# Optimization experiments

Hardware: AMD Instinct MI355X
Metric: run time of the kernel (lower is better)

The kernel has to match this reference:

```python
import jax, jax.numpy as jnp
import numpy as np

N_NODES = 50000
N_EDGES = 800000
D_FEAT = 64
THETA = [0.5, 0.3, 0.15, 0.05]  # polynomial filter coefficients, k = len(THETA)


def setup_inputs() -> dict:
    key = jax.random.key(0)
    k1, k2, k3 = jax.random.split(key, 3)
    feat = jax.random.normal(k1, (N_NODES, D_FEAT), dtype=jnp.float32)
    src = jax.random.randint(k2, (N_EDGES,), 0, N_NODES)  # A[src, dst] = 1
    dst = jax.random.randint(k3, (N_EDGES,), 0, N_NODES)
    return {"feat": feat, "src": src, "dst": dst}


def reference(feat, src, dst):
    # normalize_adj: D^{-1/2} A^T D^{-1/2} with D = rowsum(A) (inf -> 0 for isolated nodes).
    n = feat.shape[0]
    deg = jax.ops.segment_sum(jnp.ones(src.shape, dtype=feat.dtype), src, num_segments=n)
    d_inv_sqrt = jnp.where(deg > 0, jax.lax.rsqrt(jnp.maximum(deg, 1.0)), jnp.zeros_like(deg))
    # norm[i, j] = d_i^{-1/2} A[j, i] d_j^{-1/2}; edge (src=j, dst=i) carries weight
    w = d_inv_sqrt[src] * d_inv_sqrt[dst]  # [E]

    def spmm(x):
        # (A_norm @ x)[i] = sum over edges with dst==i of w_e * x[src_e]
        return jax.ops.segment_sum(w[:, None] * x[src], dst, num_segments=n)

    # Original loop: h = theta[0]*(A@f); for k>=1: f = A@f; h += theta[k]*f.
    # Note theta[0] and theta[1] both scale A@f0 (feat is not updated before h init),
    # so we fold them together and avoid recomputing the first SpMM.
    x = spmm(feat)  # A @ f0, shared by the k=0 and k=1 terms
    h = (THETA[0] + THETA[1]) * x
    for k in range(2, len(THETA)):
        x = spmm(x)
        h = h + THETA[k] * x
    return h
```

## Files before the change

kernel.cpp:

```cpp
#include <hip/hip_runtime.h>
#include <hip/hip_bf16.h>

#define N_NODES 50000
#define N_EDGES 800000
#define D_FEAT  64
#define NW      12500
#define G_SRC   64
#define G_DST   256
#define CONV_NB 128
#define FILL_NB 64
#define HB      512
#define SCAN_B  256
#define SCAN_NBLK ((NW + SCAN_B - 1) / SCAN_B)
#define CAP     48


typedef unsigned uint4_ev  __attribute__((ext_vector_type(4)));
typedef float    float4_ev __attribute__((ext_vector_type(4)));

__device__ __forceinline__ float bflo(unsigned u) { return __uint_as_float(u << 16); }
__device__ __forceinline__ float bfhi(unsigned u) { return __uint_as_float(u & 0xFFFF0000u); }
__device__ __forceinline__ unsigned pack_bf16(float a, float b) {
    __hip_bfloat16 x = __float2bfloat16(a), y = __float2bfloat16(b);
    unsigned short ux = *reinterpret_cast<unsigned short*>(&x);
    unsigned short uy = *reinterpret_cast<unsigned short*>(&y);
    return (unsigned)ux | ((unsigned)uy << 16);
}


__global__ void hist_cv_kernel(const int* __restrict__ src, const int* __restrict__ dst,
                               unsigned* __restrict__ psrc_p, unsigned* __restrict__ pdst_p,
                               const float* __restrict__ feat, unsigned* __restrict__ featbf,
                               unsigned* __restrict__ csr, int nE) {
    int t = threadIdx.x;
    int b = blockIdx.x;
    if (b >= G_SRC + G_DST + CONV_NB) {
        int fb = b - (G_SRC + G_DST + CONV_NB);
        uint4* c4 = (uint4*)csr;
        const int n4 = N_NODES * CAP / 4;
        const int nthr = FILL_NB * HB;
        uint4 z = make_uint4(0u, 0u, 0u, 0u);
        for (int i = fb * HB + t; i < n4; i += nthr) c4[i] = z;
        return;
    }
    if (b >= G_SRC + G_DST) {
        int cb = b - (G_SRC + G_DST);
        const float4* f4 = (const float4*)feat;
        uint2* fb2 = (uint2*)featbf;
        const int nthr = CONV_NB * HB;
        for (int i = cb * HB + t; i < N_NODES * 16; i += nthr) {
            float4 v = f4[i];
            fb2[i] = make_uint2(pack_bf16(v.x, v.y), pack_bf16(v.z, v.w));
        }
        return;
    }
    __shared__ unsigned bins[NW];
    for (int i = t; i < NW; i += HB) bins[i] = 0;
    __syncthreads();
    bool is_src = (b < G_SRC);
    int g = is_src ? b : (b - G_SRC);
    int nstr = is_src ? G_SRC : G_DST;
    const int4* k4 = (const int4*)(is_src ? src : dst);
    int nE4 = nE >> 2;
    for (int q = g * HB + t; q < nE4; q += nstr * HB) {
        int4 kv = k4[q];
        atomicAdd(&bins[kv.x >> 2], 1u << (8 * (kv.x & 3)));
        atomicAdd(&bins[kv.y >> 2], 1u << (8 * (kv.y & 3)));
        atomicAdd(&bins[kv.z >> 2], 1u << (8 * (kv.z & 3)));
        atomicAdd(&bins[kv.w >> 2], 1u << (8 * (kv.w & 3)));
    }
    __syncthreads();
    unsigned* p = (is_src ? psrc_p : pdst_p) + g * NW;
    for (int i = t; i < NW; i += HB) p[i] = bins[i];
}

__global__ void scanA_kernel(const unsigned* __restrict__ pdst_p, const unsigned* __restrict__ psrc_p,
                             unsigned* __restrict__ gbase_p, unsigned* __restrict__ deg_p,
                             float* __restrict__ dinv) {
    int w = blockIdx.x * SCAN_B + threadIdx.x;
    if (w >= NW) return;
    unsigned td = 0;
    #pragma unroll 16
    for (int g = 0; g < G_DST; g++) {
        gbase_p[g * NW + w] = td;
        td += pdst_p[g * NW + w];
    }
    deg_p[w] = td;
    unsigned ts = 0;
    #pragma unroll 16
    for (int g = 0; g < G_SRC; g++) ts += psrc_p[g * NW + w];
    unsigned d0 = ts & 255u, d1 = (ts >> 8) & 255u, d2 = (ts >> 16) & 255u, d3 = ts >> 24;
    float4 dv;
    dv.x = d0 ? rsqrtf((float)d0) : 0.0f;
    dv.y = d1 ? rsqrtf((float)d1) : 0.0f;
    dv.z = d2 ? rsqrtf((float)d2) : 0.0f;
    dv.w = d3 ? rsqrtf((float)d3) : 0.0f;
    ((float4*)dinv)[w] = dv;
}

__global__ void scatter_kernel(const int* __restrict__ src, const int* __restrict__ dst,
                               const unsigned* __restrict__ gbase_p, const float* __restrict__ dinv,
                               unsigned* __restrict__ csr, int nE) {
    __shared__ unsigned cur[NW];
    int t = threadIdx.x;
    int g = blockIdx.x;
    const unsigned* gb = gbase_p + (size_t)g * NW;
    for (int i = t; i < NW; i += HB) cur[i] = gb[i];
    __syncthreads();
    const int4* s4 = (const int4*)src;
    const int4* d4 = (const int4*)dst;
    int nE4 = nE >> 2;
    for (int q = g * HB + t; q < nE4; q += G_DST * HB) {
        int4 sv = s4[q];
        int4 dv = d4[q];
        {
            int k = dv.x; int sh = 8 * (k & 3);
            unsigned old = atomicAdd(&cur[k >> 2], 1u << sh);
            unsigned pw = __float2uint_rn(dinv[sv.x] * 32767.0f);
            csr[(size_t)k * CAP + ((old >> sh) & 255u)] = (pw << 17) | (unsigned)sv.x;
        }
        {
            int k = dv.y; int sh = 8 * (k & 3);
            unsigned old = atomicAdd(&cur[k >> 2], 1u << sh);
            unsigned pw = __float2uint_rn(dinv[sv.y] * 32767.0f);
            csr[(size_t)k * CAP + ((old >> sh) & 255u)] = (pw << 17) | (unsigned)sv.y;
        }
        {
            int k = dv.z; int sh = 8 * (k & 3);
            unsigned old = atomicAdd(&cur[k >> 2], 1u << sh);
            unsigned pw = __float2uint_rn(dinv[sv.z] * 32767.0f);
            csr[(size_t)k * CAP + ((old >> sh) & 255u)] = (pw << 17) | (unsigned)sv.z;
        }
        {
            int k = dv.w; int sh = 8 * (k & 3);
            unsigned old = atomicAdd(&cur[k >> 2], 1u << sh);
            unsigned pw = __float2uint_rn(dinv[sv.w] * 32767.0f);
            csr[(size_t)k * CAP + ((old >> sh) & 255u)] = (pw << 17) | (unsigned)sv.w;
        }
    }
}


struct Acc8 { float a0, a1, a2, a3, a4, a5, a6, a7; };

__device__ __forceinline__ Acc8 spmm_gather(int i, const unsigned* __restrict__ csr,
                                            const unsigned* __restrict__ x, unsigned deg,
                                            int eg, int c8) {
    const unsigned* row = csr + (size_t)i * CAP;
    const uint4* x4 = (const uint4*)x;
    const float WS = 1.0f / 32767.0f;
    unsigned v0 = __builtin_nontemporal_load(row + eg);
    unsigned v1 = __builtin_nontemporal_load(row + eg + 8);
    unsigned v2 = __builtin_nontemporal_load(row + eg + 16);
    int   s0 = (int)(v0 & 0x1FFFFu); float w0 = (float)(v0 >> 17) * WS;
    int   s1 = (int)(v1 & 0x1FFFFu); float w1 = (float)(v1 >> 17) * WS;
    int   s2 = (int)(v2 & 0x1FFFFu); float w2 = (float)(v2 >> 17) * WS;
    uint4 r0 = x4[(size_t)s0 * 8 + c8];
    uint4 r1 = x4[(size_t)s1 * 8 + c8];
    uint4 r2 = x4[(size_t)s2 * 8 + c8];
    float a0, a1, a2, a3, a4, a5, a6, a7;
    a0  = w0 * bflo(r0.x) + w1 * bflo(r1.x) + w2 * bflo(r2.x);
    a1  = w0 * bfhi(r0.x) + w1 * bfhi(r1.x) + w2 * bfhi(r2.x);
    a2  = w0 * bflo(r0.y) + w1 * bflo(r1.y) + w2 * bflo(r2.y);
    a3  = w0 * bfhi(r0.y) + w1 * bfhi(r1.y) + w2 * bfhi(r2.y);
    a4  = w0 * bflo(r0.z) + w1 * bflo(r1.z) + w2 * bflo(r2.z);
    a5  = w0 * bfhi(r0.z) + w1 * bfhi(r1.z) + w2 * bfhi(r2.z);
    a6  = w0 * bflo(r0.w) + w1 * bflo(r1.w) + w2 * bflo(r2.w);
    a7  = w0 * bfhi(r0.w) + w1 * bfhi(r1.w) + w2 * bfhi(r2.w);
    if (deg > 24) {
        unsigned v3 = __builtin_nontemporal_load(row + eg + 24);
        unsigned v4 = __builtin_nontemporal_load(row + eg + 32);
        unsigned v5 = __builtin_nontemporal_load(row + eg + 40);
        int   s3 = (int)(v3 & 0x1FFFFu); float w3 = (float)(v3 >> 17) * WS;
        int   s4 = (int)(v4 & 0x1FFFFu); float w4 = (float)(v4 >> 17) * WS;
        int   s5 = (int)(v5 & 0x1FFFFu); float w5 = (float)(v5 >> 17) * WS;
        uint4 r3 = x4[(size_t)s3 * 8 + c8];
        uint4 r4 = x4[(size_t)s4 * 8 + c8];
        uint4 r5 = x4[(size_t)s5 * 8 + c8];
        a0 += w3 * bflo(r3.x) + w4 * bflo(r4.x) + w5 * bflo(r5.x);
        a1 += w3 * bfhi(r3.x) + w4 * bfhi(r4.x) + w5 * bfhi(r5.x);
        a2 += w3 * bflo(r3.y) + w4 * bflo(r4.y) + w5 * bflo(r5.y);
        a3 += w3 * bfhi(r3.y) + w4 * bfhi(r4.y) + w5 * bfhi(r5.y);
        a4 += w3 * bflo(r3.z) + w4 * bflo(r4.z) + w5 * bflo(r5.z);
        a5 += w3 * bfhi(r3.z) + w4 * bfhi(r4.z) + w5 * bfhi(r5.z);
        a6 += w3 * bflo(r3.w) + w4 * bflo(r4.w) + w5 * bflo(r5.w);
        a7 += w3 * bfhi(r3.w) + w4 * bfhi(r4.w) + w5 * bfhi(r5.w);
    }
    #pragma unroll
    for (int d = 8; d <= 32; d <<= 1) {
        a0 += __shfl_xor(a0, d); a1 += __shfl_xor(a1, d);
        a2 += __shfl_xor(a2, d); a3 += __shfl_xor(a3, d);
        a4 += __shfl_xor(a4, d); a5 += __shfl_xor(a5, d);
        a6 += __shfl_xor(a6, d); a7 += __shfl_xor(a7, d);
    }
    Acc8 r = {a0, a1, a2, a3, a4, a5, a6, a7};
    return r;
}

__device__ __forceinline__ unsigned get_deg(const unsigned* __restrict__ deg_p, int i) {
    return (deg_p[(unsigned)i >> 2] >> (8 * (i & 3))) & 255u;
}

__global__ void spmm_mid_kernel(const unsigned* __restrict__ csr, const unsigned* __restrict__ deg_p,
                                const float* __restrict__ dinv,
                                const unsigned* __restrict__ x, unsigned* __restrict__ y) {
    int i = (blockIdx.x * blockDim.x + threadIdx.x) >> 6;
    if (i >= N_NODES) return;
    int lane = threadIdx.x & 63;
    unsigned deg = get_deg(deg_p, i);
    Acc8 A = spmm_gather(i, csr, x, deg, lane >> 3, lane & 7);
    if (lane < 8) {
        float di = dinv[i];
        uint4_ev p;
        p.x = pack_bf16(A.a0 * di, A.a1 * di);
        p.y = pack_bf16(A.a2 * di, A.a3 * di);
        p.z = pack_bf16(A.a4 * di, A.a5 * di);
        p.w = pack_bf16(A.a6 * di, A.a7 * di);
        __builtin_nontemporal_store(p, (uint4_ev*)y + (size_t)i * 8 + lane);
    }
}

__global__ void spmm_final_kernel(const unsigned* __restrict__ csr, const unsigned* __restrict__ deg_p,
                                  const float* __restrict__ dinv,
                                  const unsigned* __restrict__ x1, const unsigned* __restrict__ x2,
                                  float* __restrict__ h) {
    int i = (blockIdx.x * blockDim.x + threadIdx.x) >> 6;
    if (i >= N_NODES) return;
    int lane = threadIdx.x & 63;
    unsigned deg = get_deg(deg_p, i);
    Acc8 A = spmm_gather(i, csr, x2, deg, lane >> 3, lane & 7);
    if (lane < 8) {
        int c8 = lane;
        float di = dinv[i] * 0.05f;
        uint4 u1 = ((const uint4*)x1)[(size_t)i * 8 + c8];
        uint4 u2 = ((const uint4*)x2)[(size_t)i * 8 + c8];
        float4_ev o0, o1;
        o0.x = 0.8f * bflo(u1.x) + 0.15f * bflo(u2.x) + di * A.a0;
        o0.y = 0.8f * bfhi(u1.x) + 0.15f * bfhi(u2.x) + di * A.a1;
        o0.z = 0.8f * bflo(u1.y) + 0.15f * bflo(u2.y) + di * A.a2;
        o0.w = 0.8f * bfhi(u1.y) + 0.15f * bfhi(u2.y) + di * A.a3;
        o1.x = 0.8f * bflo(u1.z) + 0.15f * bflo(u2.z) + di * A.a4;
        o1.y = 0.8f * bfhi(u1.z) + 0.15f * bfhi(u2.z) + di * A.a5;
        o1.z = 0.8f * bflo(u1.w) + 0.15f * bflo(u2.w) + di * A.a6;
        o1.w = 0.8f * bfhi(u1.w) + 0.15f * bfhi(u2.w) + di * A.a7;
        float* hp = h + (size_t)i * 64 + c8 * 8;
        __builtin_nontemporal_store(o0, (float4_ev*)hp);
        __builtin_nontemporal_store(o1, (float4_ev*)(hp + 4));
    }
}


extern "C" void kernel_launch(void* const* d_in, const int* in_sizes, int n_in,
                              void* d_out, int out_size, void* d_ws, size_t ws_size,
                              hipStream_t stream) {
    const float* feat = (const float*)d_in[0];
    const int*   src  = (const int*)d_in[1];
    const int*   dst  = (const int*)d_in[2];
    float* h = (float*)d_out;

    char* ws = (char*)d_ws;
    unsigned* psrc_p   = (unsigned*)(ws);
    unsigned* pdst_p   = (unsigned*)(ws +  3200000u);
    unsigned* gbase_p  = (unsigned*)(ws + 16000000u);
    float*    dinv     = (float*)   (ws + 28800000u);
    unsigned* csr      = (unsigned*)(ws + 29000192u);
    unsigned* featbf   = (unsigned*)(ws + 38600192u);
    unsigned* bufA     = (unsigned*)(ws + 45000192u);
    unsigned* bufB     = (unsigned*)(ws + 51400192u);
    unsigned* deg_p    = (unsigned*)(ws + 57800192u);

    const int nE = N_EDGES;
    const int B = 256;

    hist_cv_kernel<<<G_SRC + G_DST + CONV_NB + FILL_NB, HB, 0, stream>>>(
        src, dst, psrc_p, pdst_p, feat, featbf, csr, nE);

    scanA_kernel<<<SCAN_NBLK, SCAN_B, 0, stream>>>(pdst_p, psrc_p, gbase_p, deg_p, dinv);

    scatter_kernel<<<G_DST, HB, 0, stream>>>(src, dst, gbase_p, dinv, csr, nE);

    const int spmmGrid = (N_NODES * 64 + B - 1) / B;
    spmm_mid_kernel<<<spmmGrid, B, 0, stream>>>(csr, deg_p, dinv, featbf, bufA);
    spmm_mid_kernel<<<spmmGrid, B, 0, stream>>>(csr, deg_p, dinv, bufA, bufB);
    spmm_final_kernel<<<spmmGrid, B, 0, stream>>>(csr, deg_p, dinv, bufA, bufB, h);
}
```

Baseline: 160.0 us.

## Map eight rows per wavefront with serial edge loop instead of one row

```diff
diff --git a/kernel.cpp b/kernel.cpp
--- a/kernel.cpp
+++ b/kernel.cpp
@@ -141,82 +141,67 @@
 }
 
 
+__device__ __forceinline__ unsigned get_deg(const unsigned* __restrict__ deg_p, int i) {
+    return (deg_p[(unsigned)i >> 2] >> (8 * (i & 3))) & 255u;
+}
+
 struct Acc8 { float a0, a1, a2, a3, a4, a5, a6, a7; };
 
-__device__ __forceinline__ Acc8 spmm_gather(int i, const unsigned* __restrict__ csr,
-                                            const unsigned* __restrict__ x, unsigned deg,
-                                            int eg, int c8) {
-    const unsigned* row = csr + (size_t)i * CAP;
+__device__ __forceinline__ Acc8 spmm_accum(int ii, int mdr, const unsigned* __restrict__ csr,
+                                           const unsigned* __restrict__ x, int c8) {
+    const unsigned* row = csr + (size_t)ii * CAP;
     const uint4* x4 = (const uint4*)x;
     const float WS = 1.0f / 32767.0f;
-    unsigned v0 = __builtin_nontemporal_load(row + eg);
-    unsigned v1 = __builtin_nontemporal_load(row + eg + 8);
-    unsigned v2 = __builtin_nontemporal_load(row + eg + 16);
-    int   s0 = (int)(v0 & 0x1FFFFu); float w0 = (float)(v0 >> 17) * WS;
-    int   s1 = (int)(v1 & 0x1FFFFu); float w1 = (float)(v1 >> 17) * WS;
-    int   s2 = (int)(v2 & 0x1FFFFu); float w2 = (float)(v2 >> 17) * WS;
-    uint4 r0 = x4[(size_t)s0 * 8 + c8];
-    uint4 r1 = x4[(size_t)s1 * 8 + c8];
-    uint4 r2 = x4[(size_t)s2 * 8 + c8];
-    float a0, a1, a2, a3, a4, a5, a6, a7;
-    a0  = w0 * bflo(r0.x) + w1 * bflo(r1.x) + w2 * bflo(r2.x);
-    a1  = w0 * bfhi(r0.x) + w1 * bfhi(r1.x) + w2 * bfhi(r2.x);
-    a2  = w0 * bflo(r0.y) + w1 * bflo(r1.y) + w2 * bflo(r2.y);
-    a3  = w0 * bfhi(r0.y) + w1 * bfhi(r1.y) + w2 * bfhi(r2.y);
-    a4  = w0 * bflo(r0.z) + w1 * bflo(r1.z) + w2 * bflo(r2.z);
-    a5  = w0 * bfhi(r0.z) + w1 * bfhi(r1.z) + w2 * bfhi(r2.z);
-    a6  = w0 * bflo(r0.w) + w1 * bflo(r1.w) + w2 * bflo(r2.w);
-    a7  = w0 * bfhi(r0.w) + w1 * bfhi(r1.w) + w2 * bfhi(r2.w);
-    if (deg > 24) {
-        unsigned v3 = __builtin_nontemporal_load(row + eg + 24);
-        unsigned v4 = __builtin_nontemporal_load(row + eg + 32);
-        unsigned v5 = __builtin_nontemporal_load(row + eg + 40);
+    float a0 = 0, a1 = 0, a2 = 0, a3 = 0, a4 = 0, a5 = 0, a6 = 0, a7 = 0;
+    for (int s = 0; s < mdr; s += 4) {
+        unsigned v0 = __builtin_nontemporal_load(row + s);
+        unsigned v1 = __builtin_nontemporal_load(row + s + 1);
+        unsigned v2 = __builtin_nontemporal_load(row + s + 2);
+        unsigned v3 = __builtin_nontemporal_load(row + s + 3);
+        int   s0 = (int)(v0 & 0x1FFFFu); float w0 = (float)(v0 >> 17) * WS;
+        int   s1 = (int)(v1 & 0x1FFFFu); float w1 = (float)(v1 >> 17) * WS;
+        int   s2 = (int)(v2 & 0x1FFFFu); float w2 = (float)(v2 >> 17) * WS;
         int   s3 = (int)(v3 & 0x1FFFFu); float w3 = (float)(v3 >> 17) * WS;
-        int   s4 = (int)(v4 & 0x1FFFFu); float w4 = (float)(v4 >> 17) * WS;
-        int   s5 = (int)(v5 & 0x1FFFFu); float w5 = (float)(v5 >> 17) * WS;
+        uint4 r0 = x4[(size_t)s0 * 8 + c8];
+        uint4 r1 = x4[(size_t)s1 * 8 + c8];
+        uint4 r2 = x4[(size_t)s2 * 8 + c8];
         uint4 r3 = x4[(size_t)s3 * 8 + c8];
-        uint4 r4 = x4[(size_t)s4 * 8 + c8];
-        uint4 r5 = x4[(size_t)s5 * 8 + c8];
-        a0 += w3 * bflo(r3.x) + w4 * bflo(r4.x) + w5 * bflo(r5.x);
-        a1 += w3 * bfhi(r3.x) + w4 * bfhi(r4.x) + w5 * bfhi(r5.x);
-        a2 += w3 * bflo(r3.y) + w4 * bflo(r4.y) + w5 * bflo(r5.y);
-        a3 += w3 * bfhi(r3.y) + w4 * bfhi(r4.y) + w5 * bfhi(r5.y);
-        a4 += w3 * bflo(r3.z) + w4 * bflo(r4.z) + w5 * bflo(r5.z);
-        a5 += w3 * bfhi(r3.z) + w4 * bfhi(r4.z) + w5 * bfhi(r5.z);
-        a6 += w3 * bflo(r3.w) + w4 * bflo(r4.w) + w5 * bflo(r5.w);
-        a7 += w3 * bfhi(r3.w) + w4 * bfhi(r4.w) + w5 * bfhi(r5.w);
-    }
-    #pragma unroll
-    for (int d = 8; d <= 32; d <<= 1) {
-        a0 += __shfl_xor(a0, d); a1 += __shfl_xor(a1, d);
-        a2 += __shfl_xor(a2, d); a3 += __shfl_xor(a3, d);
-        a4 += __shfl_xor(a4, d); a5 += __shfl_xor(a5, d);
-        a6 += __shfl_xor(a6, d); a7 += __shfl_xor(a7, d);
+        a0 += w0 * bflo(r0.x) + w1 * bflo(r1.x) + w2 * bflo(r2.x) + w3 * bflo(r3.x);
+        a1 += w0 * bfhi(r0.x) + w1 * bfhi(r1.x) + w2 * bfhi(r2.x) + w3 * bfhi(r3.x);
+        a2 += w0 * bflo(r0.y) + w1 * bflo(r1.y) + w2 * bflo(r2.y) + w3 * bflo(r3.y);
+        a3 += w0 * bfhi(r0.y) + w1 * bfhi(r1.y) + w2 * bfhi(r2.y) + w3 * bfhi(r3.y);
+        a4 += w0 * bflo(r0.z) + w1 * bflo(r1.z) + w2 * bflo(r2.z) + w3 * bflo(r3.z);
+        a5 += w0 * bfhi(r0.z) + w1 * bfhi(r1.z) + w2 * bfhi(r2.z) + w3 * bfhi(r3.z);
+        a6 += w0 * bflo(r0.w) + w1 * bflo(r1.w) + w2 * bflo(r2.w) + w3 * bflo(r3.w);
+        a7 += w0 * bfhi(r0.w) + w1 * bfhi(r1.w) + w2 * bfhi(r2.w) + w3 * bfhi(r3.w);
     }
     Acc8 r = {a0, a1, a2, a3, a4, a5, a6, a7};
     return r;
-}
-
-__device__ __forceinline__ unsigned get_deg(const unsigned* __restrict__ deg_p, int i) {
-    return (deg_p[(unsigned)i >> 2] >> (8 * (i & 3))) & 255u;
 }
 
 __global__ void spmm_mid_kernel(const unsigned* __restrict__ csr, const unsigned* __restrict__ deg_p,
                                 const float* __restrict__ dinv,
                                 const unsigned* __restrict__ x, unsigned* __restrict__ y) {
-    int i = (blockIdx.x * blockDim.x + threadIdx.x) >> 6;
-    if (i >= N_NODES) return;
+    int tid = blockIdx.x * blockDim.x + threadIdx.x;
     int lane = threadIdx.x & 63;
-    unsigned deg = get_deg(deg_p, i);
-    Acc8 A = spmm_gather(i, csr, x, deg, lane >> 3, lane & 7);
-    if (lane < 8) {
+    int g = lane >> 3, c8 = lane & 7;
+    int i = (tid >> 6) * 8 + g;
+    bool valid = i < N_NODES;
+    int ii = valid ? i : 0;
+    int md = valid ? (int)get_deg(deg_p, ii) : 0;
+    md = max(md, __shfl_xor(md, 8));
+    md = max(md, __shfl_xor(md, 16));
+    md = max(md, __shfl_xor(md, 32));
+    int mdr = (md + 3) & ~3;
+    Acc8 A = spmm_accum(ii, mdr, csr, x, c8);
+    if (valid) {
         float di = dinv[i];
         uint4_ev p;
         p.x = pack_bf16(A.a0 * di, A.a1 * di);
         p.y = pack_bf16(A.a2 * di, A.a3 * di);
         p.z = pack_bf16(A.a4 * di, A.a5 * di);
         p.w = pack_bf16(A.a6 * di, A.a7 * di);
-        __builtin_nontemporal_store(p, (uint4_ev*)y + (size_t)i * 8 + lane);
+        __builtin_nontemporal_store(p, (uint4_ev*)y + (size_t)i * 8 + c8);
     }
 }
 
@@ -224,13 +209,19 @@
                                   const float* __restrict__ dinv,
                                   const unsigned* __restrict__ x1, const unsigned* __restrict__ x2,
                                   float* __restrict__ h) {
-    int i = (blockIdx.x * blockDim.x + threadIdx.x) >> 6;
-    if (i >= N_NODES) return;
+    int tid = blockIdx.x * blockDim.x + threadIdx.x;
     int lane = threadIdx.x & 63;
-    unsigned deg = get_deg(deg_p, i);
-    Acc8 A = spmm_gather(i, csr, x2, deg, lane >> 3, lane & 7);
-    if (lane < 8) {
-        int c8 = lane;
+    int g = lane >> 3, c8 = lane & 7;
+    int i = (tid >> 6) * 8 + g;
+    bool valid = i < N_NODES;
+    int ii = valid ? i : 0;
+    int md = valid ? (int)get_deg(deg_p, ii) : 0;
+    md = max(md, __shfl_xor(md, 8));
+    md = max(md, __shfl_xor(md, 16));
+    md = max(md, __shfl_xor(md, 32));
+    int mdr = (md + 3) & ~3;
+    Acc8 A = spmm_accum(ii, mdr, csr, x2, c8);
+    if (valid) {
         float di = dinv[i] * 0.05f;
         uint4 u1 = ((const uint4*)x1)[(size_t)i * 8 + c8];
         uint4 u2 = ((const uint4*)x2)[(size_t)i * 8 + c8];
@@ -279,7 +270,7 @@
 
     scatter_kernel<<<G_DST, HB, 0, stream>>>(src, dst, gbase_p, dinv, csr, nE);
 
-    const int spmmGrid = (N_NODES * 64 + B - 1) / B;
+    const int spmmGrid = (N_NODES * 8 + B - 1) / B;
     spmm_mid_kernel<<<spmmGrid, B, 0, stream>>>(csr, deg_p, dinv, featbf, bufA);
     spmm_mid_kernel<<<spmmGrid, B, 0, stream>>>(csr, deg_p, dinv, bufA, bufB);
     spmm_final_kernel<<<spmmGrid, B, 0, stream>>>(csr, deg_p, dinv, bufA, bufB, h);
```

New measurement: 159.2 us. No clear change (-0.5%).
